# Kernel tuning notes

Measured on AMD Instinct MI355X. Metric: run time of the kernel, lower is better.

## Reference

```python
import jax, jax.numpy as jnp
import numpy as np

B, N, C, H = 8, 2048, 2048, 16


def setup_inputs() -> dict:
    key = jax.random.key(0)
    k1, k2, k3, k4 = jax.random.split(key, 4)
    x = jax.random.normal(k1, (B, N, C), dtype=jnp.float32)
    W_attn = jax.random.normal(k2, (C, C), dtype=jnp.float32) * 0.02
    W_proj = jax.random.normal(k3, (C, C), dtype=jnp.float32) * 0.02
    temp = jnp.ones((H, 1), dtype=jnp.float32)
    denom_bias = jax.random.normal(k4, (H, N, 1), dtype=jnp.float32) * 0.01
    return {"x": x, "W_attn": W_attn, "W_proj": W_proj, "temp": temp, "denom_bias": denom_bias}


def reference(x, W_attn, W_proj, temp, denom_bias):
    # x: (B, N, C); dropout layers are identity in eval mode.
    b, n, c = x.shape
    h = temp.shape[0]
    d = c // h
    eps = jnp.float32(jnp.finfo(jnp.float16).eps)  # fp16 eps used by the original

    # w: (B, H, N, D)
    w = jnp.einsum('bnc,oc->bno', x, W_attn).reshape(b, n, h, d).transpose(0, 2, 1, 3)
    w_sq = w * w

    # cumulative per-feature normalization along sequence
    denom = jnp.maximum(jnp.cumsum(w_sq, axis=2), eps)              # (B,H,N,D)
    w_normed = w_sq / denom + denom_bias[None, :, :n, :]            # (B,H,N,D)

    tmp = jnp.sum(w_normed, axis=-1) * temp[None]                   # (B,H,N), temp (H,1) broadcasts over N
    Pi = jax.nn.softmax(tmp, axis=1)                                # softmax over heads

    # second cumulative scan weighted by Pi
    dots = jnp.cumsum(w_sq * Pi[..., None], axis=2) / (jnp.cumsum(Pi, axis=-1) + eps)[..., None]
    attn = 1.0 / (1.0 + dots)                                       # (B,H,N,D)

    y = -(w * Pi[..., None]) * attn                                 # (B,H,N,D)
    y = y.transpose(0, 2, 1, 3).reshape(b, n, c)                    # (B,N,C)
    return jnp.einsum('bnc,oc->bno', y, W_proj)
```

## Files before the change

kernel.cpp:

```cpp
#include <hip/hip_runtime.h>
#include <math.h>

typedef _Float16 f16;
typedef f16 f16x8 __attribute__((ext_vector_type(8)));
typedef float f32x4 __attribute__((ext_vector_type(4)));

#define EPS_F16 0.0009765625f


__global__ __launch_bounds__(256) void k_cast_all(const float* __restrict__ x,
                                                  const float* __restrict__ Wa,
                                                  const float* __restrict__ Wp,
                                                  f16* __restrict__ xh,
                                                  f16* __restrict__ Wah,
                                                  f16* __restrict__ Wpb) {
  long long i = (long long)blockIdx.x * blockDim.x + threadIdx.x;
  const float* src;
  f16* dst;
  long long off;
  if (i < 4194304LL) { src = x;  dst = xh;  off = i; }
  else if (i < 4718592LL) { src = Wa; dst = Wah; off = i - 4194304LL; }
  else { src = Wp; dst = Wpb; off = i - 4718592LL; }
  const float4* in4 = (const float4*)src;
  float4 a = in4[off * 2];
  float4 b = in4[off * 2 + 1];
  f16x8 o;
  o[0] = (f16)a.x; o[1] = (f16)a.y; o[2] = (f16)a.z; o[3] = (f16)a.w;
  o[4] = (f16)b.x; o[5] = (f16)b.y; o[6] = (f16)b.z; o[7] = (f16)b.w;
  *(f16x8*)(dst + off * 8) = o;
}

__device__ __forceinline__ void gl2lds16(const void* g, void* l) {
  __builtin_amdgcn_global_load_lds(
      (const __attribute__((address_space(1))) void*)g,
      (__attribute__((address_space(3))) void*)l, 16, 0, 0);
}

template <int VM>
__device__ __forceinline__ void wait_vm() {
  if constexpr (VM == 8)      asm volatile("s_waitcnt vmcnt(8)" ::: "memory");
  else if constexpr (VM == 4) asm volatile("s_waitcnt vmcnt(4)" ::: "memory");
  else                        asm volatile("s_waitcnt vmcnt(0)" ::: "memory");
  __builtin_amdgcn_sched_barrier(0);
}

__device__ __forceinline__ void pipe_barrier() {
  __builtin_amdgcn_sched_barrier(0);
  asm volatile("" ::: "memory");
  __builtin_amdgcn_s_barrier();
  asm volatile("" ::: "memory");
  __builtin_amdgcn_sched_barrier(0);
}

template <int MODE>
__global__ __launch_bounds__(512, 2) void gemm256(const f16* __restrict__ A,
                                                  const f16* __restrict__ Bm,
                                                  float* __restrict__ Cout,
                                                  f16* __restrict__ Wout,
                                                  float* __restrict__ psum) {
  constexpr int K = 2048;
  constexpr int NT = K / 32;
  __shared__ alignas(16) char lds[131072];
  const int t = threadIdx.x;
  const int lane = t & 63;
  const int wid = t >> 6;
  const int wm = wid >> 2;
  const int wn = wid & 3;

  const int lin = blockIdx.y * 8 + blockIdx.x;
  const int logical = (lin & 7) * 64 + (lin >> 3);
  const size_t bm = (size_t)(logical >> 3) * 256;
  const size_t bn = (size_t)(logical & 7) * 256;

  const int sk = ((t & 3) * 8) ^ (((t >> 5) & 1) << 4);
  size_t aOff[2], bOff[2];
#pragma unroll
  for (int j = 0; j < 2; ++j) {
    int sr = j * 128 + (t >> 6) * 16 + ((t & 63) >> 2);
    aOff[j] = (bm + (size_t)sr) * K + sk;
    bOff[j] = (bn + (size_t)sr) * K + sk;
  }
  const int t16 = t * 16;

  const int lbyte = (((lane & 15) * 64 + (lane >> 4) * 16) ^ ((lane & 8) << 2));

  f32x4 acc[8][4] = {};

  auto stage_tile = [&](int kt) {
    char* base = lds + (kt & 3) * 32768;
    const size_t ko = (size_t)kt * 32;
#pragma unroll
    for (int j = 0; j < 2; ++j) {
      gl2lds16(A + aOff[j] + ko, base + j * 8192 + t16);
      gl2lds16(Bm + bOff[j] + ko, base + 16384 + j * 8192 + t16);
    }
  };

  auto compute_tile = [&](int slot) {
    const char* Ab = lds + slot * 32768 + wm * 8192 + lbyte;
    const char* Bb = lds + slot * 32768 + 16384 + wn * 4096 + lbyte;
    f16x8 bfr[4];
#pragma unroll
    for (int fj = 0; fj < 4; ++fj) bfr[fj] = *(const f16x8*)(Bb + fj * 1024);
#pragma unroll
    for (int q = 0; q < 4; ++q) {
      f16x8 af0 = *(const f16x8*)(Ab + (q * 2) * 1024);
      f16x8 af1 = *(const f16x8*)(Ab + (q * 2 + 1) * 1024);
      __builtin_amdgcn_s_setprio(1);
#pragma unroll
      for (int fj = 0; fj < 4; ++fj) {
        acc[q * 2][fj] = __builtin_amdgcn_mfma_f32_16x16x32_f16(
            af0, bfr[fj], acc[q * 2][fj], 0, 0, 0);
        acc[q * 2 + 1][fj] = __builtin_amdgcn_mfma_f32_16x16x32_f16(
            af1, bfr[fj], acc[q * 2 + 1][fj], 0, 0, 0);
      }
      __builtin_amdgcn_s_setprio(0);
    }
  };

  stage_tile(0);
  stage_tile(1);
  stage_tile(2);
  wait_vm<8>();
  pipe_barrier();

  for (int kt = 0; kt <= NT - 4; ++kt) {
    stage_tile(kt + 3);
    compute_tile(kt & 3);
    wait_vm<8>();
    pipe_barrier();
  }
  compute_tile((NT - 3) & 3); wait_vm<4>(); pipe_barrier();
  compute_tile((NT - 2) & 3); wait_vm<0>(); pipe_barrier();
  compute_tile((NT - 1) & 3); pipe_barrier();

  const int col = lane & 15;
  const int rb = (lane >> 4) * 4;
  if constexpr (MODE == 0) {
#pragma unroll
    for (int fi = 0; fi < 8; ++fi)
#pragma unroll
      for (int fj = 0; fj < 4; ++fj)
#pragma unroll
        for (int r = 0; r < 4; ++r) {
          size_t gr = bm + wm * 128 + fi * 16 + rb + r;
          size_t gc = bn + wn * 64 + fj * 16 + col;
          Cout[gr * 2048 + gc] = acc[fi][fj][r];
        }
  } else {
    char* W = lds + wid * 16384;
#pragma unroll
    for (int fj = 0; fj < 4; ++fj) {
      float ss = 0.f;
#pragma unroll
      for (int fi = 0; fi < 8; ++fi)
#pragma unroll
        for (int r = 0; r < 4; ++r) {
          int row_l = fi * 16 + rb + r;
          int d_l = fj * 16 + col;
          f16 q = (f16)acc[fi][fj][r];
          *(f16*)(W + row_l * 128 +
                  ((d_l * 2) ^ (((row_l >> 2) & 3) << 5))) = q;
          float qf = (float)q;
          ss += qf * qf;
        }
      ss += __shfl_xor(ss, 16);
      ss += __shfl_xor(ss, 32);
      if (lane < 16) {
        int b = (int)(bm >> 11);
        int h = (int)(bn >> 7) + (wn >> 1);
        int chunk = (int)((bm & 2047) >> 7) + wm;
        int d = (wn & 1) * 64 + fj * 16 + lane;
        psum[(((size_t)(b * 16 + h)) * 16 + chunk) * 128 + d] = ss;
      }
    }
    asm volatile("s_waitcnt lgkmcnt(0)" ::: "memory");
    __builtin_amdgcn_sched_barrier(0);
#pragma unroll
    for (int it = 0; it < 16; ++it) {
      int row_l = it * 8 + (lane >> 3);
      int g2 = (row_l >> 2) & 3;
      int c_p = lane & 7;
      f16x8 v = *(const f16x8*)(W + row_l * 128 + ((c_p * 16) ^ (g2 << 5)));
      size_t gr = bm + wm * 128 + row_l;
      int h = (int)(bn >> 7) + (wn >> 1);
      int d = (wn & 1) * 64 + c_p * 8;
      *(f16x8*)(Wout + (((gr >> 11) * 16 + h) * 2048 + (gr & 2047)) * 128 + d) =
          v;
    }
  }
}

__global__ __launch_bounds__(128) void k_tmp(const f16* __restrict__ w,
                                             const float* __restrict__ psum,
                                             const float* __restrict__ dbias,
                                             const float* __restrict__ temp,
                                             float* __restrict__ tmp) {
  __shared__ float ratio[32 * 129];
  __shared__ float part[2][32];
  int blk = blockIdx.x;
  int bh = blk >> 4, chunk = blk & 15;
  int h = bh & 15;
  int d = threadIdx.x;
  float cum = 0.f;
  for (int c = 0; c < chunk; ++c)
    cum += psum[((size_t)bh * 16 + c) * 128 + d];
  const f16* base =
      w + ((size_t)bh * 2048 + (size_t)chunk * 128) * 128 + d;
  const float tb = temp[h];
  const int r = d & 31;
  const int q = d >> 5;
#pragma unroll
  for (int s = 0; s < 4; ++s) {
    for (int i = 0; i < 32; ++i) {
      float v = (float)base[(size_t)(s * 32 + i) * 128];
      float sq = v * v;
      cum += sq;
      ratio[i * 129 + d] = sq / fmaxf(cum, EPS_F16);
    }
    __syncthreads();
    float p = 0.f;
#pragma unroll
    for (int j = 0; j < 32; ++j) p += ratio[r * 129 + q * 32 + j];
    p += __shfl_xor(p, 32);
    if ((d & 32) == 0) part[d >> 6][r] = p;
    __syncthreads();
    if (d < 32) {
      float tot = part[0][d] + part[1][d];
      int n = chunk * 128 + s * 32 + d;
      tmp[(size_t)bh * 2048 + n] = (tot + 128.f * dbias[h * 2048 + n]) * tb;
    }
    __syncthreads();
  }
}

__global__ __launch_bounds__(128) void k_partial2(const f16* __restrict__ w,
                                                  const float* __restrict__ tmp,
                                                  float* __restrict__ psum2,
                                                  float* __restrict__ pisum) {
  __shared__ float Pi_loc[128];
  int blk = blockIdx.x;
  int bh = blk >> 4, chunk = blk & 15;
  int b = bh >> 4, h = bh & 15;
  int d = threadIdx.x;
  {
    int tid = threadIdx.x;
    int n = chunk * 128 + tid;
    float v[16];
    float mx = -1e30f;
#pragma unroll
    for (int hh = 0; hh < 16; ++hh) {
      v[hh] = tmp[((size_t)(b * 16 + hh)) * 2048 + n];
      mx = fmaxf(mx, v[hh]);
    }
    float s = 0.f;
#pragma unroll
    for (int hh = 0; hh < 16; ++hh) {
      v[hh] = expf(v[hh] - mx);
      s += v[hh];
    }
    Pi_loc[tid] = v[h] * (1.f / s);
  }
  __syncthreads();
  const f16* base =
      w + ((size_t)bh * 2048 + (size_t)chunk * 128) * 128 + d;
  float s = 0.f, sp = 0.f;
#pragma unroll 4
  for (int i = 0; i < 128; ++i) {
    float p = Pi_loc[i];
    float v = (float)base[(size_t)i * 128];
    s += v * v * p;
    sp += p;
  }
  psum2[(size_t)blk * 128 + d] = s;
  if (d == 0) pisum[blk] = sp;
}

__global__ __launch_bounds__(128) void k_y(const f16* __restrict__ w,
                                           const float* __restrict__ tmp,
                                           const float* __restrict__ psum2,
                                           const float* __restrict__ pisum,
                                           f16* __restrict__ yout) {
  __shared__ float Pi_loc[128];
  int blk = blockIdx.x;
  int bh = blk >> 4, chunk = blk & 15;
  int b = bh >> 4, h = bh & 15;
  int d = threadIdx.x;
  {
    int tid = threadIdx.x;
    int n = chunk * 128 + tid;
    float v[16];
    float mx = -1e30f;
#pragma unroll
    for (int hh = 0; hh < 16; ++hh) {
      v[hh] = tmp[((size_t)(b * 16 + hh)) * 2048 + n];
      mx = fmaxf(mx, v[hh]);
    }
    float s = 0.f;
#pragma unroll
    for (int hh = 0; hh < 16; ++hh) {
      v[hh] = expf(v[hh] - mx);
      s += v[hh];
    }
    Pi_loc[tid] = v[h] * (1.f / s);
  }
  __syncthreads();
  float cum = 0.f, cpi = 0.f;
  for (int c = 0; c < chunk; ++c) {
    cum += psum2[((size_t)bh * 16 + c) * 128 + d];
    cpi += pisum[bh * 16 + c];
  }
  const f16* base =
      w + ((size_t)bh * 2048 + (size_t)chunk * 128) * 128 + d;
  for (int i = 0; i < 128; ++i) {
    float p = Pi_loc[i];
    float v = (float)base[(size_t)i * 128];
    cum += v * v * p;
    cpi += p;
    float dots = cum / (cpi + EPS_F16);
    float attn = 1.f / (1.f + dots);
    float y = -(v * p) * attn;
    int n = chunk * 128 + i;
    yout[((size_t)(b * 2048 + n)) * 2048 + h * 128 + d] = (f16)y;
  }
}

extern "C" void kernel_launch(void* const* d_in, const int* in_sizes, int n_in,
                              void* d_out, int out_size, void* d_ws, size_t ws_size,
                              hipStream_t stream) {
  const float* x     = (const float*)d_in[0];
  const float* Wa    = (const float*)d_in[1];
  const float* Wp    = (const float*)d_in[2];
  const float* temp  = (const float*)d_in[3];
  const float* dbias = (const float*)d_in[4];
  float* out = (float*)d_out;

  char* ws = (char*)d_ws;
  constexpr size_t OFF_W   = 0;
  constexpr size_t OFF_XH  = 67108864;
  constexpr size_t OFF_WAH = OFF_XH + 67108864;
  constexpr size_t OFF_WPB = OFF_WAH + 8388608;
  constexpr size_t OFF_TMP = OFF_WPB + 8388608;
  constexpr size_t OFF_PS  = OFF_TMP + 2097152;
  constexpr size_t OFF_PIS = OFF_PS + 1048576;

  f16*   w    = (f16*)(ws + OFF_W);
  f16*   xh   = (f16*)(ws + OFF_XH);
  f16*   Wah  = (f16*)(ws + OFF_WAH);
  f16*   Wpb  = (f16*)(ws + OFF_WPB);
  float* tmp  = (float*)(ws + OFF_TMP);
  float* psum = (float*)(ws + OFF_PS);
  float* pis  = (float*)(ws + OFF_PIS);

  k_cast_all<<<20480, 256, 0, stream>>>(x, Wa, Wp, xh, Wah, Wpb);

  gemm256<1><<<dim3(8, 64), 512, 0, stream>>>(xh, Wah, nullptr, w, psum);

  k_tmp<<<2048, 128, 0, stream>>>(w, psum, dbias, temp, tmp);

  k_partial2<<<2048, 128, 0, stream>>>(w, tmp, psum, pis);
  k_y<<<2048, 128, 0, stream>>>(w, tmp, psum, pis, xh);

  gemm256<0><<<dim3(8, 64), 512, 0, stream>>>(xh, Wpb, out, nullptr, nullptr);
}
```

Baseline: 400.4 us.

## Fuse fp32-to-fp16 cast of x into the first GEMM's A-tile loading

The separate cast pass over the large activation x is removed. The first GEMM now loads fp32 A tiles into registers, converts them to fp16 and writes them to LDS double-buffered, while B still streams through global_load_lds with a 4-slot ring. This saves a full read and write round trip of x through HBM, at the cost of register-path loads and cast ALU work inside the GEMM main loop, plus a more fragile pipeline with extra waitcnt stages.

```diff
diff --git a/kernel.cpp b/kernel.cpp
--- a/kernel.cpp
+++ b/kernel.cpp
@@ -8,19 +8,16 @@
 #define EPS_F16 0.0009765625f
 
 
-__global__ __launch_bounds__(256) void k_cast_all(const float* __restrict__ x,
-                                                  const float* __restrict__ Wa,
-                                                  const float* __restrict__ Wp,
-                                                  f16* __restrict__ xh,
-                                                  f16* __restrict__ Wah,
-                                                  f16* __restrict__ Wpb) {
+__global__ __launch_bounds__(256) void k_cast_w(const float* __restrict__ Wa,
+                                                const float* __restrict__ Wp,
+                                                f16* __restrict__ Wah,
+                                                f16* __restrict__ Wpb) {
   long long i = (long long)blockIdx.x * blockDim.x + threadIdx.x;
   const float* src;
   f16* dst;
   long long off;
-  if (i < 4194304LL) { src = x;  dst = xh;  off = i; }
-  else if (i < 4718592LL) { src = Wa; dst = Wah; off = i - 4194304LL; }
-  else { src = Wp; dst = Wpb; off = i - 4718592LL; }
+  if (i < 524288LL) { src = Wa; dst = Wah; off = i; }
+  else { src = Wp; dst = Wpb; off = i - 524288LL; }
   const float4* in4 = (const float4*)src;
   float4 a = in4[off * 2];
   float4 b = in4[off * 2 + 1];
@@ -39,7 +36,9 @@
 template <int VM>
 __device__ __forceinline__ void wait_vm() {
   if constexpr (VM == 8)      asm volatile("s_waitcnt vmcnt(8)" ::: "memory");
+  else if constexpr (VM == 6) asm volatile("s_waitcnt vmcnt(6)" ::: "memory");
   else if constexpr (VM == 4) asm volatile("s_waitcnt vmcnt(4)" ::: "memory");
+  else if constexpr (VM == 2) asm volatile("s_waitcnt vmcnt(2)" ::: "memory");
   else                        asm volatile("s_waitcnt vmcnt(0)" ::: "memory");
   __builtin_amdgcn_sched_barrier(0);
 }
@@ -52,12 +51,9 @@
   __builtin_amdgcn_sched_barrier(0);
 }
 
-template <int MODE>
-__global__ __launch_bounds__(512, 2) void gemm256(const f16* __restrict__ A,
+__global__ __launch_bounds__(512, 2) void gemm_bt(const f16* __restrict__ A,
                                                   const f16* __restrict__ Bm,
-                                                  float* __restrict__ Cout,
-                                                  f16* __restrict__ Wout,
-                                                  float* __restrict__ psum) {
+                                                  float* __restrict__ Cout) {
   constexpr int K = 2048;
   constexpr int NT = K / 32;
   __shared__ alignas(16) char lds[131072];
@@ -81,7 +77,6 @@
     bOff[j] = (bn + (size_t)sr) * K + sk;
   }
   const int t16 = t * 16;
-
   const int lbyte = (((lane & 15) * 64 + (lane >> 4) * 16) ^ ((lane & 8) << 2));
 
   f32x4 acc[8][4] = {};
@@ -136,58 +131,165 @@
 
   const int col = lane & 15;
   const int rb = (lane >> 4) * 4;
-  if constexpr (MODE == 0) {
+#pragma unroll
+  for (int fi = 0; fi < 8; ++fi)
+#pragma unroll
+    for (int fj = 0; fj < 4; ++fj)
+#pragma unroll
+      for (int r = 0; r < 4; ++r) {
+        size_t gr = bm + wm * 128 + fi * 16 + rb + r;
+        size_t gc = bn + wn * 64 + fj * 16 + col;
+        Cout[gr * 2048 + gc] = acc[fi][fj][r];
+      }
+}
+
+__global__ __launch_bounds__(512, 2) void gemm_x32(const float* __restrict__ A,
+                                                   const f16* __restrict__ Bm,
+                                                   f16* __restrict__ Wout,
+                                                   float* __restrict__ psum) {
+  constexpr int K = 2048;
+  constexpr int NT = K / 32;
+  __shared__ alignas(16) char lds[131072];
+  const int t = threadIdx.x;
+  const int lane = t & 63;
+  const int wid = t >> 6;
+  const int wm = wid >> 2;
+  const int wn = wid & 3;
+
+  const int lin = blockIdx.y * 8 + blockIdx.x;
+  const int logical = (lin & 7) * 64 + (lin >> 3);
+  const size_t bm = (size_t)(logical >> 3) * 256;
+  const size_t bn = (size_t)(logical & 7) * 256;
+
+  const int sk = ((t & 3) * 8) ^ (((t >> 5) & 1) << 4);
+  size_t aOff[2], bOff[2];
+#pragma unroll
+  for (int j = 0; j < 2; ++j) {
+    int sr = j * 128 + (t >> 6) * 16 + ((t & 63) >> 2);
+    aOff[j] = (bm + (size_t)sr) * K + sk;
+    bOff[j] = (bn + (size_t)sr) * K + sk;
+  }
+  const int t16 = t * 16;
+  const int lbyte = (((lane & 15) * 64 + (lane >> 4) * 16) ^ ((lane & 8) << 2));
+
+  f32x4 acc[8][4] = {};
+  float4 ar[2][2];
+
+  auto loadA = [&](int kt) {
+    const size_t ko = (size_t)kt * 32;
+#pragma unroll
+    for (int j = 0; j < 2; ++j) {
+      ar[j][0] = *(const float4*)(A + aOff[j] + ko);
+      ar[j][1] = *(const float4*)(A + aOff[j] + ko + 4);
+    }
+  };
+  auto writeA = [&](int kt) {
+    char* base = lds + (kt & 1) * 16384;
+#pragma unroll
+    for (int j = 0; j < 2; ++j) {
+      f16x8 o;
+      o[0] = (f16)ar[j][0].x; o[1] = (f16)ar[j][0].y;
+      o[2] = (f16)ar[j][0].z; o[3] = (f16)ar[j][0].w;
+      o[4] = (f16)ar[j][1].x; o[5] = (f16)ar[j][1].y;
+      o[6] = (f16)ar[j][1].z; o[7] = (f16)ar[j][1].w;
+      *(f16x8*)(base + j * 8192 + t16) = o;
+    }
+  };
+  auto stageB = [&](int kt) {
+    char* base = lds + 32768 + (kt & 3) * 16384;
+    const size_t ko = (size_t)kt * 32;
+#pragma unroll
+    for (int j = 0; j < 2; ++j)
+      gl2lds16(Bm + bOff[j] + ko, base + j * 8192 + t16);
+  };
+  auto compute_tile = [&](int kt) {
+    const char* Ab = lds + (kt & 1) * 16384 + wm * 8192 + lbyte;
+    const char* Bb = lds + 32768 + (kt & 3) * 16384 + wn * 4096 + lbyte;
+    f16x8 bfr[4];
+#pragma unroll
+    for (int fj = 0; fj < 4; ++fj) bfr[fj] = *(const f16x8*)(Bb + fj * 1024);
+#pragma unroll
+    for (int q = 0; q < 4; ++q) {
+      f16x8 af0 = *(const f16x8*)(Ab + (q * 2) * 1024);
+      f16x8 af1 = *(const f16x8*)(Ab + (q * 2 + 1) * 1024);
+      __builtin_amdgcn_s_setprio(1);
+#pragma unroll
+      for (int fj = 0; fj < 4; ++fj) {
+        acc[q * 2][fj] = __builtin_amdgcn_mfma_f32_16x16x32_f16(
+            af0, bfr[fj], acc[q * 2][fj], 0, 0, 0);
+        acc[q * 2 + 1][fj] = __builtin_amdgcn_mfma_f32_16x16x32_f16(
+            af1, bfr[fj], acc[q * 2 + 1][fj], 0, 0, 0);
+      }
+      __builtin_amdgcn_s_setprio(0);
+    }
+  };
+
+  loadA(0);
+  __builtin_amdgcn_sched_barrier(0);
+  stageB(0); stageB(1); stageB(2);
+  wait_vm<6>();
+  writeA(0);
+  loadA(1);
+  wait_vm<8>();
+  asm volatile("s_waitcnt lgkmcnt(0)" ::: "memory");
+  __builtin_amdgcn_sched_barrier(0);
+  pipe_barrier();
+
+  for (int kt = 0; kt < NT; ++kt) {
+    if (kt + 3 < NT) stageB(kt + 3);
+    compute_tile(kt);
+    if (kt + 1 < NT) {
+      if (kt + 3 < NT) wait_vm<2>();
+      else wait_vm<0>();
+      writeA(kt + 1);
+      if (kt + 2 < NT) loadA(kt + 2);
+      asm volatile("s_waitcnt lgkmcnt(0)" ::: "memory");
+      __builtin_amdgcn_sched_barrier(0);
+    }
+    pipe_barrier();
+  }
+
+  const int col = lane & 15;
+  const int rb = (lane >> 4) * 4;
+  char* W = lds + wid * 16384;
+#pragma unroll
+  for (int fj = 0; fj < 4; ++fj) {
+    float ss = 0.f;
 #pragma unroll
     for (int fi = 0; fi < 8; ++fi)
 #pragma unroll
-      for (int fj = 0; fj < 4; ++fj)
-#pragma unroll
-        for (int r = 0; r < 4; ++r) {
-          size_t gr = bm + wm * 128 + fi * 16 + rb + r;
-          size_t gc = bn + wn * 64 + fj * 16 + col;
-          Cout[gr * 2048 + gc] = acc[fi][fj][r];
-        }
-  } else {
-    char* W = lds + wid * 16384;
-#pragma unroll
-    for (int fj = 0; fj < 4; ++fj) {
-      float ss = 0.f;
-#pragma unroll
-      for (int fi = 0; fi < 8; ++fi)
-#pragma unroll
-        for (int r = 0; r < 4; ++r) {
-          int row_l = fi * 16 + rb + r;
-          int d_l = fj * 16 + col;
-          f16 q = (f16)acc[fi][fj][r];
-          *(f16*)(W + row_l * 128 +
-                  ((d_l * 2) ^ (((row_l >> 2) & 3) << 5))) = q;
-          float qf = (float)q;
-          ss += qf * qf;
-        }
-      ss += __shfl_xor(ss, 16);
-      ss += __shfl_xor(ss, 32);
-      if (lane < 16) {
-        int b = (int)(bm >> 11);
-        int h = (int)(bn >> 7) + (wn >> 1);
-        int chunk = (int)((bm & 2047) >> 7) + wm;
-        int d = (wn & 1) * 64 + fj * 16 + lane;
-        psum[(((size_t)(b * 16 + h)) * 16 + chunk) * 128 + d] = ss;
+      for (int r = 0; r < 4; ++r) {
+        int row_l = fi * 16 + rb + r;
+        int d_l = fj * 16 + col;
+        f16 q = (f16)acc[fi][fj][r];
+        *(f16*)(W + row_l * 128 +
+                ((d_l * 2) ^ (((row_l >> 2) & 3) << 5))) = q;
+        float qf = (float)q;
+        ss += qf * qf;
       }
-    }
-    asm volatile("s_waitcnt lgkmcnt(0)" ::: "memory");
-    __builtin_amdgcn_sched_barrier(0);
-#pragma unroll
-    for (int it = 0; it < 16; ++it) {
-      int row_l = it * 8 + (lane >> 3);
-      int g2 = (row_l >> 2) & 3;
-      int c_p = lane & 7;
-      f16x8 v = *(const f16x8*)(W + row_l * 128 + ((c_p * 16) ^ (g2 << 5)));
-      size_t gr = bm + wm * 128 + row_l;
+    ss += __shfl_xor(ss, 16);
+    ss += __shfl_xor(ss, 32);
+    if (lane < 16) {
+      int b = (int)(bm >> 11);
       int h = (int)(bn >> 7) + (wn >> 1);
-      int d = (wn & 1) * 64 + c_p * 8;
-      *(f16x8*)(Wout + (((gr >> 11) * 16 + h) * 2048 + (gr & 2047)) * 128 + d) =
-          v;
-    }
+      int chunk = (int)((bm & 2047) >> 7) + wm;
+      int d = (wn & 1) * 64 + fj * 16 + lane;
+      psum[(((size_t)(b * 16 + h)) * 16 + chunk) * 128 + d] = ss;
+    }
+  }
+  asm volatile("s_waitcnt lgkmcnt(0)" ::: "memory");
+  __builtin_amdgcn_sched_barrier(0);
+#pragma unroll
+  for (int it = 0; it < 16; ++it) {
+    int row_l = it * 8 + (lane >> 3);
+    int g2 = (row_l >> 2) & 3;
+    int c_p = lane & 7;
+    f16x8 v = *(const f16x8*)(W + row_l * 128 + ((c_p * 16) ^ (g2 << 5)));
+    size_t gr = bm + wm * 128 + row_l;
+    int h = (int)(bn >> 7) + (wn >> 1);
+    int d = (wn & 1) * 64 + c_p * 8;
+    *(f16x8*)(Wout + (((gr >> 11) * 16 + h) * 2048 + (gr & 2047)) * 128 + d) =
+        v;
   }
 }
 
@@ -337,29 +439,29 @@
 
   char* ws = (char*)d_ws;
   constexpr size_t OFF_W   = 0;
-  constexpr size_t OFF_XH  = 67108864;
-  constexpr size_t OFF_WAH = OFF_XH + 67108864;
+  constexpr size_t OFF_Y   = 67108864;
+  constexpr size_t OFF_WAH = OFF_Y + 67108864;
   constexpr size_t OFF_WPB = OFF_WAH + 8388608;
   constexpr size_t OFF_TMP = OFF_WPB + 8388608;
   constexpr size_t OFF_PS  = OFF_TMP + 2097152;
   constexpr size_t OFF_PIS = OFF_PS + 1048576;
 
   f16*   w    = (f16*)(ws + OFF_W);
-  f16*   xh   = (f16*)(ws + OFF_XH);
+  f16*   y    = (f16*)(ws + OFF_Y);
   f16*   Wah  = (f16*)(ws + OFF_WAH);
   f16*   Wpb  = (f16*)(ws + OFF_WPB);
   float* tmp  = (float*)(ws + OFF_TMP);
   float* psum = (float*)(ws + OFF_PS);
   float* pis  = (float*)(ws + OFF_PIS);
 
-  k_cast_all<<<20480, 256, 0, stream>>>(x, Wa, Wp, xh, Wah, Wpb);
-
-  gemm256<1><<<dim3(8, 64), 512, 0, stream>>>(xh, Wah, nullptr, w, psum);
+  k_cast_w<<<4096, 256, 0, stream>>>(Wa, Wp, Wah, Wpb);
+
+  gemm_x32<<<dim3(8, 64), 512, 0, stream>>>(x, Wah, w, psum);
 
   k_tmp<<<2048, 128, 0, stream>>>(w, psum, dbias, temp, tmp);
 
   k_partial2<<<2048, 128, 0, stream>>>(w, tmp, psum, pis);
-  k_y<<<2048, 128, 0, stream>>>(w, tmp, psum, pis, xh);
-
-  gemm256<0><<<dim3(8, 64), 512, 0, stream>>>(xh, Wpb, out, nullptr, nullptr);
-}
+  k_y<<<2048, 128, 0, stream>>>(w, tmp, psum, pis, y);
+
+  gemm_bt<<<dim3(8, 64), 512, 0, stream>>>(y, Wpb, out);
+}
```

New measurement: 441.7 us. +10.3%, slower.
